# Optimization experiments

Hardware: AMD Instinct MI355X
Metric: run time of the kernel (lower is better)

The kernel has to match this reference:

```python
import jax, jax.numpy as jnp
import numpy as np

EPS = 1e-8


def _three_nn_interpolate(coords, ref_coords, features):
    # coords: [B, N, 3], ref_coords: [B, M, 3], features: [B, C, M]
    # squared pairwise distances [B, N, M]
    d2 = (
        jnp.sum(coords * coords, axis=-1, keepdims=True)          # [B, N, 1]
        + jnp.sum(ref_coords * ref_coords, axis=-1)[:, None, :]    # [B, 1, M]
        - 2.0 * jnp.einsum('bnd,bmd->bnm', coords, ref_coords)
    )
    neg_d, idx = jax.lax.top_k(-d2, 3)       # 3 nearest -> idx [B, N, 3]
    dist = -neg_d                             # squared dists of 3-NN
    w = 1.0 / (dist + EPS)
    w = w / jnp.sum(w, axis=-1, keepdims=True)  # [B, N, 3]
    feats_t = jnp.swapaxes(features, 1, 2)    # [B, M, C]
    gathered = jax.vmap(lambda f, i: f[i])(feats_t, idx)  # [B, N, 3, C]
    out = jnp.einsum('bnk,bnkc->bcn', w, gathered)         # [B, C, N]
    return out


def setup_inputs() -> dict:
    key = jax.random.key(0)
    ks = jax.random.split(key, 5)
    B, N, M = 2, 16384, 4096
    return {
        'coords': jax.random.normal(ks[0], (B, N, 3), dtype=jnp.float32),
        'ref_coords': jax.random.normal(ks[1], (B, M, 3), dtype=jnp.float32),
        'ref_features': jax.random.normal(ks[2], (B, 256, M), dtype=jnp.float32),
        'ref_t_embed': jax.random.normal(ks[3], (B, 128, M), dtype=jnp.float32),
        'points_features': jax.random.normal(ks[4], (B, 64, N), dtype=jnp.float32),
    }


def reference(coords, ref_coords, ref_features, ref_t_embed, points_features):
    # PointNetFPModule.forward: interpolate features and t_embed from the
    # coarse ref point set onto the dense point set, then concat skip features.
    features = _three_nn_interpolate(coords, ref_coords, ref_features)  # [B, 256, N]
    t_embed = _three_nn_interpolate(coords, ref_coords, ref_t_embed)    # [B, 128, N]
    features = jnp.concatenate([features, points_features], axis=1)     # [B, 320, N]
    return features, t_embed
```

## Files before the change

### kernel.cpp

```cpp
#include <hip/hip_runtime.h>
#include <cstdint>

#define BB 2
#define NN 16384
#define MM 4096
#define CF 256
#define CT 128
#define CP 64

#define TPB1 512
#define NPB1 32
#define CHUNK 2048

__global__ __launch_bounds__(TPB1, 8) void knn_kernel(
    const float* __restrict__ coords,
    const float* __restrict__ ref_coords,
    int4* __restrict__ wsI,
    float4* __restrict__ wsW)
{
#pragma clang fp contract(off)
    __shared__ float4 refs[CHUNK];

    const int tid = threadIdx.x;
    const int b   = blockIdx.y;
    const int n0  = blockIdx.x * NPB1;

    const int pl = tid >> 4;
    const int s  = tid & 15;
    const int n  = n0 + pl;

    const float* cp = coords + ((size_t)b * NN + n) * 3;
    const float cx = cp[0];
    const float cy = cp[1];
    const float cz = cp[2];
    const float cc = (cx * cx + cy * cy) + cz * cz;

    float d0 = INFINITY, d1 = INFINITY, d2v = INFINITY;
    int   i0 = 0, i1 = 0, i2 = 0;
    float tau = INFINITY;
    float thr = INFINITY;

    const float* rc = ref_coords + (size_t)b * MM * 3;

    auto upd = [&](float dd, int j) {
        const bool l2 = dd < d2v;
        const bool l1 = dd < d1;
        const bool l0 = dd < d0;
        i2 = l2 ? (l1 ? i1 : j) : i2;
        i1 = l1 ? (l0 ? i0 : j) : i1;
        i0 = l0 ? j : i0;
        const float n2  = __builtin_amdgcn_fmed3f(dd, d1, d2v);
        const float n1  = __builtin_amdgcn_fmed3f(dd, d0, d1);
        const float nv0 = fminf(dd, d0);
        d2v = n2; d1 = n1; d0 = nv0;
    };

    for (int ch = 0; ch < MM / CHUNK; ++ch) {
        __syncthreads();
        for (int e = tid; e < CHUNK; e += TPB1) {
            const int j = ch * CHUNK + e;
            const float x = rc[3 * j + 0];
            const float y = rc[3 * j + 1];
            const float z = rc[3 * j + 2];
            refs[e] = make_float4(x + x, y + y, z + z, (x * x + y * y) + z * z);
        }
        __syncthreads();

        const int jbase = ch * CHUNK;
        for (int seg = 0; seg < CHUNK / (16 * 32); ++seg) {
            #pragma unroll
            for (int t = 0; t < 16; ++t) {
                const int ea = s + ((seg * 32 + t * 2) << 4);
                const float4 ra = refs[ea];
                const float4 rb = refs[ea + 16];
                const float dot2a = (cx * ra.x + cy * ra.y) + cz * ra.z;
                const float dda   = (cc + ra.w) - dot2a;
                const float dot2b = (cx * rb.x + cy * rb.y) + cz * rb.z;
                const float ddb   = (cc + rb.w) - dot2b;
                if (__any(fminf(dda, ddb) < thr)) {
                    const int ja = jbase + ea;
                    upd(dda, ja);
                    upd(ddb, ja + 16);
                    thr = fminf(d2v, tau);
                }
            }
            float tt = d2v;
            tt = fminf(tt, __shfl_xor(tt, 1, 64));
            tt = fminf(tt, __shfl_xor(tt, 2, 64));
            tt = fminf(tt, __shfl_xor(tt, 4, 64));
            tt = fminf(tt, __shfl_xor(tt, 8, 64));
            tau = tt;
            thr = fminf(d2v, tau);
        }
    }

    auto ins = [&](float e, int f) {
        const bool l2 = (e < d2v) || (e == d2v && f < i2);
        const bool l1 = (e < d1)  || (e == d1  && f < i1);
        const bool l0 = (e < d0)  || (e == d0  && f < i0);
        d2v = l2 ? (l1 ? d1 : e) : d2v;  i2 = l2 ? (l1 ? i1 : f) : i2;
        d1  = l1 ? (l0 ? d0 : e) : d1;   i1 = l1 ? (l0 ? i0 : f) : i1;
        d0  = l0 ? e : d0;               i0 = l0 ? f : i0;
    };

    for (int off = 1; off < 16; off <<= 1) {
        const float e0 = __shfl_xor(d0,  off, 64);
        const float e1 = __shfl_xor(d1,  off, 64);
        const float e2 = __shfl_xor(d2v, off, 64);
        const int   f0 = __shfl_xor(i0,  off, 64);
        const int   f1 = __shfl_xor(i1,  off, 64);
        const int   f2 = __shfl_xor(i2,  off, 64);
        ins(e0, f0);
        ins(e1, f1);
        ins(e2, f2);
    }

    if (s == 0) {
        float w0 = 1.0f / (d0  + 1e-8f);
        float w1 = 1.0f / (d1  + 1e-8f);
        float w2 = 1.0f / (d2v + 1e-8f);
        const float sum = (w0 + w1) + w2;
        wsI[(size_t)b * NN + n] = make_int4(i0, i1, i2, 0);
        wsW[(size_t)b * NN + n] = make_float4(w0 / sum, w1 / sum, w2 / sum, 0.0f);
    }
}

#define TPB2 512
#define NIB  (BB * (CF + CT) / 2)
#define NCB  32

__global__ __launch_bounds__(TPB2, 8) void interp_kernel(
    const float* __restrict__ refF,
    const float* __restrict__ refT,
    const float* __restrict__ pf,
    const int4*  __restrict__ wsI,
    const float4* __restrict__ wsW,
    float* __restrict__ out)
{
#pragma clang fp contract(off)
    __shared__ float rowA[MM];
    __shared__ float rowB[MM];
    const int tid  = threadIdx.x;
    const int task = blockIdx.x;
    const size_t outT_base = (size_t)BB * (CF + CP) * NN;

    if (task >= NIB) {
        const int t3 = task - NIB;
        for (int j = 0; j < 4; ++j) {
            const int r  = t3 * 4 + j;
            const int bb = r >> 6;
            const int c  = r & (CP - 1);
            const float4* s4 = (const float4*)(pf + ((size_t)bb * CP + c) * NN);
            float4* d4 = (float4*)(out + ((size_t)bb * (CF + CP) + CF + c) * NN);
            for (int i = tid; i < NN / 4; i += TPB2) d4[i] = s4[i];
        }
        return;
    }

    const int r0 = task * 2;
    const float* src0;
    float* dst0;
    int b;
    if (r0 < BB * CF) {
        b = r0 >> 8;
        const int c = r0 & (CF - 1);
        src0 = refF + ((size_t)b * CF + c) * MM;
        dst0 = out + ((size_t)b * (CF + CP) + c) * NN;
    } else {
        const int r2 = r0 - BB * CF;
        b = r2 >> 7;
        const int c = r2 & (CT - 1);
        src0 = refT + ((size_t)b * CT + c) * MM;
        dst0 = out + outT_base + ((size_t)b * CT + c) * NN;
    }
    const float* src1 = src0 + MM;
    float* dst1 = dst0 + NN;

    for (int i = tid; i < MM / 4; i += TPB2) {
        ((float4*)rowA)[i] = ((const float4*)src0)[i];
        ((float4*)rowB)[i] = ((const float4*)src1)[i];
    }
    __syncthreads();

    const int4*   wi = wsI + (size_t)b * NN;
    const float4* ww = wsW + (size_t)b * NN;

    auto clampi = [](int v) { return v < 0 ? 0 : (v > MM - 1 ? MM - 1 : v); };

    int4   id = wi[tid];
    float4 w  = ww[tid];
    for (int nq = tid; nq < NN; nq += TPB2) {
        const int nq2 = nq + TPB2;
        int4   idn;
        float4 wn;
        if (nq2 < NN) { idn = wi[nq2]; wn = ww[nq2]; }
        const int a0 = clampi(id.x), a1 = clampi(id.y), a2 = clampi(id.z);
        dst0[nq] = (w.x * rowA[a0] + w.y * rowA[a1]) + w.z * rowA[a2];
        dst1[nq] = (w.x * rowB[a0] + w.y * rowB[a1]) + w.z * rowB[a2];
        id = idn; w = wn;
    }
}

extern "C" void kernel_launch(void* const* d_in, const int* in_sizes, int n_in,
                              void* d_out, int out_size, void* d_ws, size_t ws_size,
                              hipStream_t stream) {
    const float* coords     = (const float*)d_in[0];
    const float* ref_coords = (const float*)d_in[1];
    const float* refF       = (const float*)d_in[2];
    const float* refT       = (const float*)d_in[3];
    const float* pf         = (const float*)d_in[4];
    float* out = (float*)d_out;

    int4*   wsI = (int4*)d_ws;
    float4* wsW = (float4*)((char*)d_ws + (size_t)BB * NN * sizeof(int4));

    hipLaunchKernelGGL(knn_kernel, dim3(NN / NPB1, BB), dim3(TPB1), 0, stream,
                       coords, ref_coords, wsI, wsW);
    hipLaunchKernelGGL(interp_kernel, dim3(NIB + NCB), dim3(TPB2), 0, stream,
                       refF, refT, pf, wsI, wsW, out);
}
```

Measured before the change: 173.9 us.

## Process two query points per thread in kNN and drop wave-vote pruning

Each thread now handles two query points, so every shared-memory reference load is reused for two distance computations, and each block covers 64 points instead of 32. The per-pair __any vote and the periodic shuffle-based threshold that skipped top-3 updates are removed, so every candidate now goes through the unconditional insert. This cuts LDS traffic per distance and removes branch and shuffle overhead. In exchange it doubles the register state per thread, lowers the occupancy hint from 8 to 4, and gives up the early skipping of candidates that cannot enter the top-3.

```diff
diff --git a/kernel.cpp b/kernel.cpp
--- a/kernel.cpp
+++ b/kernel.cpp
@@ -9,10 +9,10 @@
 #define CP 64
 
 #define TPB1 512
-#define NPB1 32
+#define NPB1 64
 #define CHUNK 2048
 
-__global__ __launch_bounds__(TPB1, 8) void knn_kernel(
+__global__ __launch_bounds__(TPB1, 4) void knn_kernel(
     const float* __restrict__ coords,
     const float* __restrict__ ref_coords,
     int4* __restrict__ wsI,
@@ -27,33 +27,20 @@
 
     const int pl = tid >> 4;
     const int s  = tid & 15;
-    const int n  = n0 + pl;
-
-    const float* cp = coords + ((size_t)b * NN + n) * 3;
-    const float cx = cp[0];
-    const float cy = cp[1];
-    const float cz = cp[2];
-    const float cc = (cx * cx + cy * cy) + cz * cz;
-
-    float d0 = INFINITY, d1 = INFINITY, d2v = INFINITY;
-    int   i0 = 0, i1 = 0, i2 = 0;
-    float tau = INFINITY;
-    float thr = INFINITY;
+    const int nA = n0 + pl * 2;
+
+    const float* cp = coords + ((size_t)b * NN + nA) * 3;
+    const float ax = cp[0], ay = cp[1], az = cp[2];
+    const float bx = cp[3], by = cp[4], bz = cp[5];
+    const float acc_ = (ax * ax + ay * ay) + az * az;
+    const float bcc_ = (bx * bx + by * by) + bz * bz;
+
+    float aD0 = INFINITY, aD1 = INFINITY, aD2 = INFINITY;
+    float bD0 = INFINITY, bD1 = INFINITY, bD2 = INFINITY;
+    int   aI0 = 0, aI1 = 0, aI2 = 0;
+    int   bI0 = 0, bI1 = 0, bI2 = 0;
 
     const float* rc = ref_coords + (size_t)b * MM * 3;
-
-    auto upd = [&](float dd, int j) {
-        const bool l2 = dd < d2v;
-        const bool l1 = dd < d1;
-        const bool l0 = dd < d0;
-        i2 = l2 ? (l1 ? i1 : j) : i2;
-        i1 = l1 ? (l0 ? i0 : j) : i1;
-        i0 = l0 ? j : i0;
-        const float n2  = __builtin_amdgcn_fmed3f(dd, d1, d2v);
-        const float n1  = __builtin_amdgcn_fmed3f(dd, d0, d1);
-        const float nv0 = fminf(dd, d0);
-        d2v = n2; d1 = n1; d0 = nv0;
-    };
 
     for (int ch = 0; ch < MM / CHUNK; ++ch) {
         __syncthreads();
@@ -66,62 +53,101 @@
         }
         __syncthreads();
 
-        const int jbase = ch * CHUNK;
-        for (int seg = 0; seg < CHUNK / (16 * 32); ++seg) {
+        const float4* rp = &refs[s];
+        const int jb0 = ch * CHUNK + s;
+        for (int kb = 0; kb < CHUNK / 16 / 32; ++kb) {
+            const float4* rpb = rp + (size_t)kb * 32 * 16;
+            const int jbb = jb0 + (kb * 32) * 16;
             #pragma unroll
-            for (int t = 0; t < 16; ++t) {
-                const int ea = s + ((seg * 32 + t * 2) << 4);
-                const float4 ra = refs[ea];
-                const float4 rb = refs[ea + 16];
-                const float dot2a = (cx * ra.x + cy * ra.y) + cz * ra.z;
-                const float dda   = (cc + ra.w) - dot2a;
-                const float dot2b = (cx * rb.x + cy * rb.y) + cz * rb.z;
-                const float ddb   = (cc + rb.w) - dot2b;
-                if (__any(fminf(dda, ddb) < thr)) {
-                    const int ja = jbase + ea;
-                    upd(dda, ja);
-                    upd(ddb, ja + 16);
-                    thr = fminf(d2v, tau);
+            for (int k = 0; k < 32; ++k) {
+                const float4 r = rpb[k * 16];
+                const int j = jbb + k * 16;
+                {
+                    const float dot2 = (ax * r.x + ay * r.y) + az * r.z;
+                    const float dd   = (acc_ + r.w) - dot2;
+                    const bool l2 = dd < aD2;
+                    const bool l1 = dd < aD1;
+                    const bool l0 = dd < aD0;
+                    aI2 = l2 ? (l1 ? aI1 : j) : aI2;
+                    aI1 = l1 ? (l0 ? aI0 : j) : aI1;
+                    aI0 = l0 ? j : aI0;
+                    const float n2  = __builtin_amdgcn_fmed3f(dd, aD1, aD2);
+                    const float n1  = __builtin_amdgcn_fmed3f(dd, aD0, aD1);
+                    const float n0v = fminf(dd, aD0);
+                    aD2 = n2; aD1 = n1; aD0 = n0v;
+                }
+                {
+                    const float dot2 = (bx * r.x + by * r.y) + bz * r.z;
+                    const float dd   = (bcc_ + r.w) - dot2;
+                    const bool l2 = dd < bD2;
+                    const bool l1 = dd < bD1;
+                    const bool l0 = dd < bD0;
+                    bI2 = l2 ? (l1 ? bI1 : j) : bI2;
+                    bI1 = l1 ? (l0 ? bI0 : j) : bI1;
+                    bI0 = l0 ? j : bI0;
+                    const float n2  = __builtin_amdgcn_fmed3f(dd, bD1, bD2);
+                    const float n1  = __builtin_amdgcn_fmed3f(dd, bD0, bD1);
+                    const float n0v = fminf(dd, bD0);
+                    bD2 = n2; bD1 = n1; bD0 = n0v;
                 }
             }
-            float tt = d2v;
-            tt = fminf(tt, __shfl_xor(tt, 1, 64));
-            tt = fminf(tt, __shfl_xor(tt, 2, 64));
-            tt = fminf(tt, __shfl_xor(tt, 4, 64));
-            tt = fminf(tt, __shfl_xor(tt, 8, 64));
-            tau = tt;
-            thr = fminf(d2v, tau);
-        }
-    }
-
-    auto ins = [&](float e, int f) {
-        const bool l2 = (e < d2v) || (e == d2v && f < i2);
-        const bool l1 = (e < d1)  || (e == d1  && f < i1);
-        const bool l0 = (e < d0)  || (e == d0  && f < i0);
-        d2v = l2 ? (l1 ? d1 : e) : d2v;  i2 = l2 ? (l1 ? i1 : f) : i2;
-        d1  = l1 ? (l0 ? d0 : e) : d1;   i1 = l1 ? (l0 ? i0 : f) : i1;
-        d0  = l0 ? e : d0;               i0 = l0 ? f : i0;
-    };
+        }
+    }
 
     for (int off = 1; off < 16; off <<= 1) {
-        const float e0 = __shfl_xor(d0,  off, 64);
-        const float e1 = __shfl_xor(d1,  off, 64);
-        const float e2 = __shfl_xor(d2v, off, 64);
-        const int   f0 = __shfl_xor(i0,  off, 64);
-        const int   f1 = __shfl_xor(i1,  off, 64);
-        const int   f2 = __shfl_xor(i2,  off, 64);
-        ins(e0, f0);
-        ins(e1, f1);
-        ins(e2, f2);
+        {
+            const float e0 = __shfl_xor(aD0, off, 64);
+            const float e1 = __shfl_xor(aD1, off, 64);
+            const float e2 = __shfl_xor(aD2, off, 64);
+            const int   f0 = __shfl_xor(aI0, off, 64);
+            const int   f1 = __shfl_xor(aI1, off, 64);
+            const int   f2 = __shfl_xor(aI2, off, 64);
+            auto ins = [&](float e, int f) {
+                const bool l2 = (e < aD2) || (e == aD2 && f < aI2);
+                const bool l1 = (e < aD1) || (e == aD1 && f < aI1);
+                const bool l0 = (e < aD0) || (e == aD0 && f < aI0);
+                aD2 = l2 ? (l1 ? aD1 : e) : aD2;  aI2 = l2 ? (l1 ? aI1 : f) : aI2;
+                aD1 = l1 ? (l0 ? aD0 : e) : aD1;  aI1 = l1 ? (l0 ? aI0 : f) : aI1;
+                aD0 = l0 ? e : aD0;               aI0 = l0 ? f : aI0;
+            };
+            ins(e0, f0); ins(e1, f1); ins(e2, f2);
+        }
+        {
+            const float e0 = __shfl_xor(bD0, off, 64);
+            const float e1 = __shfl_xor(bD1, off, 64);
+            const float e2 = __shfl_xor(bD2, off, 64);
+            const int   f0 = __shfl_xor(bI0, off, 64);
+            const int   f1 = __shfl_xor(bI1, off, 64);
+            const int   f2 = __shfl_xor(bI2, off, 64);
+            auto ins = [&](float e, int f) {
+                const bool l2 = (e < bD2) || (e == bD2 && f < bI2);
+                const bool l1 = (e < bD1) || (e == bD1 && f < bI1);
+                const bool l0 = (e < bD0) || (e == bD0 && f < bI0);
+                bD2 = l2 ? (l1 ? bD1 : e) : bD2;  bI2 = l2 ? (l1 ? bI1 : f) : bI2;
+                bD1 = l1 ? (l0 ? bD0 : e) : bD1;  bI1 = l1 ? (l0 ? bI0 : f) : bI1;
+                bD0 = l0 ? e : bD0;               bI0 = l0 ? f : bI0;
+            };
+            ins(e0, f0); ins(e1, f1); ins(e2, f2);
+        }
     }
 
     if (s == 0) {
-        float w0 = 1.0f / (d0  + 1e-8f);
-        float w1 = 1.0f / (d1  + 1e-8f);
-        float w2 = 1.0f / (d2v + 1e-8f);
-        const float sum = (w0 + w1) + w2;
-        wsI[(size_t)b * NN + n] = make_int4(i0, i1, i2, 0);
-        wsW[(size_t)b * NN + n] = make_float4(w0 / sum, w1 / sum, w2 / sum, 0.0f);
+        {
+            float w0 = 1.0f / (aD0 + 1e-8f);
+            float w1 = 1.0f / (aD1 + 1e-8f);
+            float w2 = 1.0f / (aD2 + 1e-8f);
+            const float sum = (w0 + w1) + w2;
+            wsI[(size_t)b * NN + nA] = make_int4(aI0, aI1, aI2, 0);
+            wsW[(size_t)b * NN + nA] = make_float4(w0 / sum, w1 / sum, w2 / sum, 0.0f);
+        }
+        {
+            float w0 = 1.0f / (bD0 + 1e-8f);
+            float w1 = 1.0f / (bD1 + 1e-8f);
+            float w2 = 1.0f / (bD2 + 1e-8f);
+            const float sum = (w0 + w1) + w2;
+            wsI[(size_t)b * NN + nA + 1] = make_int4(bI0, bI1, bI2, 0);
+            wsW[(size_t)b * NN + nA + 1] = make_float4(w0 / sum, w1 / sum, w2 / sum, 0.0f);
+        }
     }
 }
 
```

Result: slower. 182.9 us (+5.2%).

## Split KNN chunk across two block halves with shared-memory top-3 merge

Applied to the files above, without the earlier changes.

Each query point is now handled by 8 lanes in each of two block halves, with each half scanning a different 1024-entry half of the shared reference chunk. The threshold reduction and the final shuffle merge now run over 8 lanes, and a shared-memory step merges the two halves' top-3 lists. The aim is a cheaper per-wave threshold reduction and tighter pruning because each wave covers fewer queries per lane group. The cost is one extra __syncthreads, a small shared-memory merge, and a different within-wave divergence pattern in the __any check.

```diff
diff --git a/kernel.cpp b/kernel.cpp
--- a/kernel.cpp
+++ b/kernel.cpp
@@ -11,6 +11,7 @@
 #define TPB1 512
 #define NPB1 32
 #define CHUNK 2048
+#define HALFE 1024
 
 __global__ __launch_bounds__(TPB1, 8) void knn_kernel(
     const float* __restrict__ coords,
@@ -20,13 +21,16 @@
 {
 #pragma clang fp contract(off)
     __shared__ float4 refs[CHUNK];
+    __shared__ float  mD[NPB1][2][4];
+    __shared__ int    mI[NPB1][2][4];
 
     const int tid = threadIdx.x;
     const int b   = blockIdx.y;
     const int n0  = blockIdx.x * NPB1;
 
-    const int pl = tid >> 4;
-    const int s  = tid & 15;
+    const int pl = (tid >> 3) & (NPB1 - 1);
+    const int s  = tid & 7;
+    const int h  = tid >> 8;
     const int n  = n0 + pl;
 
     const float* cp = coords + ((size_t)b * NN + n) * 3;
@@ -41,19 +45,6 @@
     float thr = INFINITY;
 
     const float* rc = ref_coords + (size_t)b * MM * 3;
-
-    auto upd = [&](float dd, int j) {
-        const bool l2 = dd < d2v;
-        const bool l1 = dd < d1;
-        const bool l0 = dd < d0;
-        i2 = l2 ? (l1 ? i1 : j) : i2;
-        i1 = l1 ? (l0 ? i0 : j) : i1;
-        i0 = l0 ? j : i0;
-        const float n2  = __builtin_amdgcn_fmed3f(dd, d1, d2v);
-        const float n1  = __builtin_amdgcn_fmed3f(dd, d0, d1);
-        const float nv0 = fminf(dd, d0);
-        d2v = n2; d1 = n1; d0 = nv0;
-    };
 
     for (int ch = 0; ch < MM / CHUNK; ++ch) {
         __syncthreads();
@@ -66,21 +57,27 @@
         }
         __syncthreads();
 
-        const int jbase = ch * CHUNK;
-        for (int seg = 0; seg < CHUNK / (16 * 32); ++seg) {
-            #pragma unroll
-            for (int t = 0; t < 16; ++t) {
-                const int ea = s + ((seg * 32 + t * 2) << 4);
-                const float4 ra = refs[ea];
-                const float4 rb = refs[ea + 16];
-                const float dot2a = (cx * ra.x + cy * ra.y) + cz * ra.z;
-                const float dda   = (cc + ra.w) - dot2a;
-                const float dot2b = (cx * rb.x + cy * rb.y) + cz * rb.z;
-                const float ddb   = (cc + rb.w) - dot2b;
-                if (__any(fminf(dda, ddb) < thr)) {
-                    const int ja = jbase + ea;
-                    upd(dda, ja);
-                    upd(ddb, ja + 16);
+        const int ebase = h * HALFE + s;
+        const int jbase = ch * CHUNK + ebase;
+        for (int it0 = 0; it0 < HALFE / 8; it0 += 32) {
+            #pragma unroll 4
+            for (int k = 0; k < 32; ++k) {
+                const int off8 = (it0 + k) << 3;
+                const float4 r = refs[ebase + off8];
+                const float dot2 = (cx * r.x + cy * r.y) + cz * r.z;
+                const float dd   = (cc + r.w) - dot2;
+                if (__any(dd < thr)) {
+                    const int j = jbase + off8;
+                    const bool l2 = dd < d2v;
+                    const bool l1 = dd < d1;
+                    const bool l0 = dd < d0;
+                    i2 = l2 ? (l1 ? i1 : j) : i2;
+                    i1 = l1 ? (l0 ? i0 : j) : i1;
+                    i0 = l0 ? j : i0;
+                    const float n2  = __builtin_amdgcn_fmed3f(dd, d1, d2v);
+                    const float n1  = __builtin_amdgcn_fmed3f(dd, d0, d1);
+                    const float n0v = fminf(dd, d0);
+                    d2v = n2; d1 = n1; d0 = n0v;
                     thr = fminf(d2v, tau);
                 }
             }
@@ -88,7 +85,6 @@
             tt = fminf(tt, __shfl_xor(tt, 1, 64));
             tt = fminf(tt, __shfl_xor(tt, 2, 64));
             tt = fminf(tt, __shfl_xor(tt, 4, 64));
-            tt = fminf(tt, __shfl_xor(tt, 8, 64));
             tau = tt;
             thr = fminf(d2v, tau);
         }
@@ -103,7 +99,7 @@
         d0  = l0 ? e : d0;               i0 = l0 ? f : i0;
     };
 
-    for (int off = 1; off < 16; off <<= 1) {
+    for (int off = 1; off < 8; off <<= 1) {
         const float e0 = __shfl_xor(d0,  off, 64);
         const float e1 = __shfl_xor(d1,  off, 64);
         const float e2 = __shfl_xor(d2v, off, 64);
@@ -116,6 +112,15 @@
     }
 
     if (s == 0) {
+        mD[pl][h][0] = d0;  mD[pl][h][1] = d1;  mD[pl][h][2] = d2v;
+        mI[pl][h][0] = i0;  mI[pl][h][1] = i1;  mI[pl][h][2] = i2;
+    }
+    __syncthreads();
+
+    if (h == 0 && s == 0) {
+        ins(mD[pl][1][0], mI[pl][1][0]);
+        ins(mD[pl][1][1], mI[pl][1][1]);
+        ins(mD[pl][1][2], mI[pl][1][2]);
         float w0 = 1.0f / (d0  + 1e-8f);
         float w1 = 1.0f / (d1  + 1e-8f);
         float w2 = 1.0f / (d2v + 1e-8f);
```

Measured after the change: 180.4 us. 3.7% more time.

## Restructure kNN to one point per lane with register-prefetched uniform refs

Applied to the files above, without the earlier changes.

Adds a prep kernel that precomputes doubled ref coords and squared norms into workspace. The kNN kernel now gives each lane a whole query point, with two waves each scanning half of the references. References are read as wave-uniform loads into double-buffered register arrays instead of shared memory. A warm-up phase runs unconditional updates, and later candidates are filtered with wave-wide __any tests before a shared-memory merge of the two halves. This removes the 16-lane shuffle reductions and LDS staging, but launches only 512 blocks of 128 threads, which risks low occupancy and more divergence.

```diff
diff --git a/kernel.cpp b/kernel.cpp
--- a/kernel.cpp
+++ b/kernel.cpp
@@ -8,26 +8,38 @@
 #define CT 128
 #define CP 64
 
-#define TPB1 512
-#define NPB1 32
-#define CHUNK 2048
-
-__global__ __launch_bounds__(TPB1, 8) void knn_kernel(
+__global__ __launch_bounds__(256) void prep_kernel(
+    const float* __restrict__ rc,
+    float4* __restrict__ wsR)
+{
+#pragma clang fp contract(off)
+    const int j = blockIdx.x * 256 + threadIdx.x;
+    if (j < BB * MM) {
+        const float x = rc[3 * j + 0];
+        const float y = rc[3 * j + 1];
+        const float z = rc[3 * j + 2];
+        wsR[j] = make_float4(x + x, y + y, z + z, (x * x + y * y) + z * z);
+    }
+}
+
+#define TPB1 128
+#define WARM 16
+
+__global__ __launch_bounds__(TPB1, 1) void knn_kernel(
     const float* __restrict__ coords,
-    const float* __restrict__ ref_coords,
+    const float4* __restrict__ wsR,
     int4* __restrict__ wsI,
     float4* __restrict__ wsW)
 {
 #pragma clang fp contract(off)
-    __shared__ float4 refs[CHUNK];
-
-    const int tid = threadIdx.x;
-    const int b   = blockIdx.y;
-    const int n0  = blockIdx.x * NPB1;
-
-    const int pl = tid >> 4;
-    const int s  = tid & 15;
-    const int n  = n0 + pl;
+    __shared__ float mD[64][3];
+    __shared__ int   mI[64][3];
+
+    const int tid  = threadIdx.x;
+    const int lane = tid & 63;
+    const int wu   = __builtin_amdgcn_readfirstlane(tid >> 6);
+    const int b    = blockIdx.y;
+    const int n    = blockIdx.x * 64 + lane;
 
     const float* cp = coords + ((size_t)b * NN + n) * 3;
     const float cx = cp[0];
@@ -37,10 +49,9 @@
 
     float d0 = INFINITY, d1 = INFINITY, d2v = INFINITY;
     int   i0 = 0, i1 = 0, i2 = 0;
-    float tau = INFINITY;
-    float thr = INFINITY;
-
-    const float* rc = ref_coords + (size_t)b * MM * 3;
+
+    const float4* rp = wsR + (size_t)b * MM + wu * (MM / 2);
+    const int jh = wu * (MM / 2);
 
     auto upd = [&](float dd, int j) {
         const bool l2 = dd < d2v;
@@ -51,71 +62,71 @@
         i0 = l0 ? j : i0;
         const float n2  = __builtin_amdgcn_fmed3f(dd, d1, d2v);
         const float n1  = __builtin_amdgcn_fmed3f(dd, d0, d1);
-        const float nv0 = fminf(dd, d0);
-        d2v = n2; d1 = n1; d0 = nv0;
+        const float n0v = fminf(dd, d0);
+        d2v = n2; d1 = n1; d0 = n0v;
     };
 
-    for (int ch = 0; ch < MM / CHUNK; ++ch) {
-        __syncthreads();
-        for (int e = tid; e < CHUNK; e += TPB1) {
-            const int j = ch * CHUNK + e;
-            const float x = rc[3 * j + 0];
-            const float y = rc[3 * j + 1];
-            const float z = rc[3 * j + 2];
-            refs[e] = make_float4(x + x, y + y, z + z, (x * x + y * y) + z * z);
-        }
-        __syncthreads();
-
-        const int jbase = ch * CHUNK;
-        for (int seg = 0; seg < CHUNK / (16 * 32); ++seg) {
+    float4 A[16], B[16];
+    #pragma unroll
+    for (int k = 0; k < 16; ++k) A[k] = rp[k];
+
+    auto step = [&](float4 (&cur)[16], float4 (&nxt)[16], const int sg) {
+        #pragma unroll
+        for (int k = 0; k < 16; ++k) nxt[k] = rp[(sg + 1) * 16 + k];
+        const int jb = jh + sg * 16;
+        if (sg < WARM) {
             #pragma unroll
-            for (int t = 0; t < 16; ++t) {
-                const int ea = s + ((seg * 32 + t * 2) << 4);
-                const float4 ra = refs[ea];
-                const float4 rb = refs[ea + 16];
-                const float dot2a = (cx * ra.x + cy * ra.y) + cz * ra.z;
-                const float dda   = (cc + ra.w) - dot2a;
-                const float dot2b = (cx * rb.x + cy * rb.y) + cz * rb.z;
-                const float ddb   = (cc + rb.w) - dot2b;
-                if (__any(fminf(dda, ddb) < thr)) {
-                    const int ja = jbase + ea;
-                    upd(dda, ja);
-                    upd(ddb, ja + 16);
-                    thr = fminf(d2v, tau);
+            for (int k = 0; k < 16; ++k) {
+                const float4 r = cur[k];
+                const float dd = (cc + r.w) - ((cx * r.x + cy * r.y) + cz * r.z);
+                upd(dd, jb + k);
+            }
+        } else {
+            #pragma unroll
+            for (int kg = 0; kg < 4; ++kg) {
+                const float4 ra = cur[kg * 4 + 0];
+                const float4 rb = cur[kg * 4 + 1];
+                const float4 rc4 = cur[kg * 4 + 2];
+                const float4 rd = cur[kg * 4 + 3];
+                const float dda = (cc + ra.w) - ((cx * ra.x + cy * ra.y) + cz * ra.z);
+                const float ddb = (cc + rb.w) - ((cx * rb.x + cy * rb.y) + cz * rb.z);
+                const float ddc = (cc + rc4.w) - ((cx * rc4.x + cy * rc4.y) + cz * rc4.z);
+                const float ddd = (cc + rd.w) - ((cx * rd.x + cy * rd.y) + cz * rd.z);
+                const float mn = fminf(fminf(dda, ddb), fminf(ddc, ddd));
+                if (__any(mn < d2v)) {
+                    if (__any(dda < d2v)) upd(dda, jb + kg * 4 + 0);
+                    if (__any(ddb < d2v)) upd(ddb, jb + kg * 4 + 1);
+                    if (__any(ddc < d2v)) upd(ddc, jb + kg * 4 + 2);
+                    if (__any(ddd < d2v)) upd(ddd, jb + kg * 4 + 3);
                 }
             }
-            float tt = d2v;
-            tt = fminf(tt, __shfl_xor(tt, 1, 64));
-            tt = fminf(tt, __shfl_xor(tt, 2, 64));
-            tt = fminf(tt, __shfl_xor(tt, 4, 64));
-            tt = fminf(tt, __shfl_xor(tt, 8, 64));
-            tau = tt;
-            thr = fminf(d2v, tau);
         }
-    }
-
-    auto ins = [&](float e, int f) {
-        const bool l2 = (e < d2v) || (e == d2v && f < i2);
-        const bool l1 = (e < d1)  || (e == d1  && f < i1);
-        const bool l0 = (e < d0)  || (e == d0  && f < i0);
-        d2v = l2 ? (l1 ? d1 : e) : d2v;  i2 = l2 ? (l1 ? i1 : f) : i2;
-        d1  = l1 ? (l0 ? d0 : e) : d1;   i1 = l1 ? (l0 ? i0 : f) : i1;
-        d0  = l0 ? e : d0;               i0 = l0 ? f : i0;
     };
 
-    for (int off = 1; off < 16; off <<= 1) {
-        const float e0 = __shfl_xor(d0,  off, 64);
-        const float e1 = __shfl_xor(d1,  off, 64);
-        const float e2 = __shfl_xor(d2v, off, 64);
-        const int   f0 = __shfl_xor(i0,  off, 64);
-        const int   f1 = __shfl_xor(i1,  off, 64);
-        const int   f2 = __shfl_xor(i2,  off, 64);
-        ins(e0, f0);
-        ins(e1, f1);
-        ins(e2, f2);
-    }
-
-    if (s == 0) {
+    for (int so = 0; so < 64; ++so) {
+        step(A, B, 2 * so);
+        step(B, A, 2 * so + 1);
+    }
+
+    if (wu == 1) {
+        mD[lane][0] = d0;  mD[lane][1] = d1;  mD[lane][2] = d2v;
+        mI[lane][0] = i0;  mI[lane][1] = i1;  mI[lane][2] = i2;
+    }
+    __syncthreads();
+
+    if (wu == 0) {
+        auto ins = [&](float e, int f) {
+            const bool l2 = (e < d2v) || (e == d2v && f < i2);
+            const bool l1 = (e < d1)  || (e == d1  && f < i1);
+            const bool l0 = (e < d0)  || (e == d0  && f < i0);
+            d2v = l2 ? (l1 ? d1 : e) : d2v;  i2 = l2 ? (l1 ? i1 : f) : i2;
+            d1  = l1 ? (l0 ? d0 : e) : d1;   i1 = l1 ? (l0 ? i0 : f) : i1;
+            d0  = l0 ? e : d0;               i0 = l0 ? f : i0;
+        };
+        ins(mD[lane][0], mI[lane][0]);
+        ins(mD[lane][1], mI[lane][1]);
+        ins(mD[lane][2], mI[lane][2]);
+
         float w0 = 1.0f / (d0  + 1e-8f);
         float w1 = 1.0f / (d1  + 1e-8f);
         float w2 = 1.0f / (d2v + 1e-8f);
@@ -211,11 +222,15 @@
     const float* pf         = (const float*)d_in[4];
     float* out = (float*)d_out;
 
-    int4*   wsI = (int4*)d_ws;
-    float4* wsW = (float4*)((char*)d_ws + (size_t)BB * NN * sizeof(int4));
-
-    hipLaunchKernelGGL(knn_kernel, dim3(NN / NPB1, BB), dim3(TPB1), 0, stream,
-                       coords, ref_coords, wsI, wsW);
+    const size_t WSR_BYTES = (size_t)(BB * MM + 16) * sizeof(float4);
+    float4* wsR = (float4*)d_ws;
+    int4*   wsI = (int4*)((char*)d_ws + WSR_BYTES);
+    float4* wsW = (float4*)((char*)d_ws + WSR_BYTES + (size_t)BB * NN * sizeof(int4));
+
+    hipLaunchKernelGGL(prep_kernel, dim3((BB * MM + 255) / 256), dim3(256), 0, stream,
+                       ref_coords, wsR);
+    hipLaunchKernelGGL(knn_kernel, dim3(NN / 64, BB), dim3(TPB1), 0, stream,
+                       coords, wsR, wsI, wsW);
     hipLaunchKernelGGL(interp_kernel, dim3(NIB + NCB), dim3(TPB2), 0, stream,
                        refF, refT, pf, wsI, wsW, out);
 }
```

Measured after the change: 324.1 us. +86.3%, slower.
